# Performance work log

Hardware: AMD Instinct MI355X
Metric: run time of the kernel (lower is better)

Reference implementation:

```python
import jax, jax.numpy as jnp
import numpy as np

NUM_HEADS = 16
HEAD_DIM = 64
MAX_REL = 128
NEG_INF = -1e30


def setup_inputs() -> dict:
    key = jax.random.key(0)
    ks = jax.random.split(key, 5)
    B, L, D = 2, 2048, 1024
    x = jax.random.normal(ks[0], (B, L, D), dtype=jnp.float32)
    key_padding_mask = jnp.zeros((B, L), dtype=bool)  # True = padded
    Wqkv = jax.random.normal(ks[1], (D, 3 * D), dtype=jnp.float32) * (D ** -0.5)
    bqkv = jnp.zeros((3 * D,), dtype=jnp.float32)
    Wout = jax.random.normal(ks[2], (D, D), dtype=jnp.float32) * (D ** -0.5)
    bout = jnp.zeros((D,), dtype=jnp.float32)
    bias_table = jax.random.normal(ks[3], (2 * MAX_REL + 1, NUM_HEADS), dtype=jnp.float32) * 0.02
    return {"x": x, "key_padding_mask": key_padding_mask, "Wqkv": Wqkv,
            "bqkv": bqkv, "Wout": Wout, "bout": bout, "bias_table": bias_table}


def _rel_bias(bias_table, L):
    # relative position index: clamp(k - q, -MAX_REL, MAX_REL) + MAX_REL -> [L, L]
    rel = jnp.arange(L)[None, :] - jnp.arange(L)[:, None]
    idx = jnp.clip(rel, -MAX_REL, MAX_REL) + MAX_REL
    return bias_table[idx].transpose(2, 0, 1)  # [H, L, L]


def reference(x, key_padding_mask, Wqkv, bqkv, Wout, bout, bias_table):
    B, L, D = x.shape
    H, hd = NUM_HEADS, HEAD_DIM
    qkv = x @ Wqkv + bqkv                      # [B, L, 3D]
    q, k, v = jnp.split(qkv, 3, axis=-1)
    q = q.reshape(B, L, H, hd).transpose(0, 2, 1, 3)  # [B, H, L, hd]
    k = k.reshape(B, L, H, hd).transpose(0, 2, 1, 3)
    v = v.reshape(B, L, H, hd).transpose(0, 2, 1, 3)
    scores = jnp.einsum('bhqd,bhkd->bhqk', q, k) * (hd ** -0.5)
    scores = scores + _rel_bias(bias_table, L)[None]   # [B, H, L, L]
    scores = jnp.where(key_padding_mask[:, None, None, :], NEG_INF, scores)
    attn = jax.nn.softmax(scores, axis=-1)
    out = jnp.einsum('bhqk,bhkd->bhqd', attn, v)       # [B, H, L, hd]
    out = out.transpose(0, 2, 1, 3).reshape(B, L, D)
    return out @ Wout + bout
```

## Files before the change

### kernel.cpp

```cpp
#include <hip/hip_runtime.h>
#include <hip/hip_bf16.h>
#include <stdint.h>

#define LSEQ 2048
#define BATCH 2
#define DMODEL 1024
#define NH 16
#define HD 64

typedef __attribute__((ext_vector_type(8))) short bf16x8;
typedef __attribute__((ext_vector_type(4))) float f32x4;

__device__ __forceinline__ short f2bf(float f) {
  union { float f; uint32_t u; } v; v.f = f;
  uint32_t r = v.u + 0x8000u;
  return (short)(r >> 16);
}

__device__ __forceinline__ uint32_t pack_bf16(float lo, float hi) {
  union { float f; uint32_t u; } a, b; a.f = lo; b.f = hi;
  uint32_t al = (a.u + 0x8000u) >> 16;
  uint32_t bh = (b.u + 0x8000u) & 0xFFFF0000u;
  return al | bh;
}

__device__ __forceinline__ float exp2_fast(float x) {
#if __has_builtin(__builtin_amdgcn_exp2f)
  return __builtin_amdgcn_exp2f(x);
#else
  float r; asm("v_exp_f32 %0, %1" : "=v"(r) : "v"(x)); return r;
#endif
}

__device__ __forceinline__ void gll16(const void* g, void* l) {
  __builtin_amdgcn_global_load_lds(
      (const __attribute__((address_space(1))) void*)g,
      (__attribute__((address_space(3))) void*)l, 16, 0, 0);
}

__global__ void cvt_bf16(const float* __restrict__ in, short* __restrict__ out, int n) {
  int i = (blockIdx.x * blockDim.x + threadIdx.x) * 4;
  if (i < n) {
    float4 v = *(const float4*)(in + i);
    short4 o;
    o.x = f2bf(v.x); o.y = f2bf(v.y); o.z = f2bf(v.z); o.w = f2bf(v.w);
    *(short4*)(out + i) = o;
  }
}

__global__ void transpose_cvt(const float* __restrict__ in, short* __restrict__ out,
                              int K, int N) {
  __shared__ float tile[32][33];
  int kb = blockIdx.x * 32, nb = blockIdx.y * 32;
  int tx = threadIdx.x & 31, ty = threadIdx.x >> 5;
  #pragma unroll
  for (int i = ty; i < 32; i += 8)
    tile[i][tx] = in[(size_t)(kb + i) * N + nb + tx];
  __syncthreads();
  #pragma unroll
  for (int i = ty; i < 32; i += 8)
    out[(size_t)(nb + i) * K + kb + tx] = f2bf(tile[tx][i]);
}

template <int EPI>
__global__ __launch_bounds__(256, 2) void gemm_bt(
    const short* __restrict__ A, const short* __restrict__ Bt,
    const float* __restrict__ bias, float* __restrict__ outf,
    short* __restrict__ q_out, short* __restrict__ k_out, short* __restrict__ v_out) {
  constexpr int K = 1024, BK = 64, NKT = K / BK;
  __shared__ short Als[2][128 * BK];
  __shared__ short Bls[2][128 * BK];
  const int tid = threadIdx.x;
  const int lane = tid & 63;
  const int c = lane & 15, g = lane >> 4;
  const int m0 = blockIdx.x * 128;
  const int n0 = blockIdx.y * 128;
  const int wid = tid >> 6;
  const int wm = (wid >> 1) * 64, wn = (wid & 1) * 64;

  f32x4 acc[4][4] = {};

  auto stage = [&](int kt, int bbuf) {
    const int k0 = kt * BK;
    #pragma unroll
    for (int inst = 0; inst < 4; ++inst) {
      int i = inst * 256 + tid;
      int row = i >> 3, cg = i & 7;
      int scc = cg ^ (row & 7);
      gll16(A + (size_t)(m0 + row) * K + k0 + scc * 8, &Als[bbuf][i * 8]);
      gll16(Bt + (size_t)(n0 + row) * K + k0 + scc * 8, &Bls[bbuf][i * 8]);
    }
  };

  stage(0, 0);

  for (int kt = 0; kt < NKT; ++kt) {
    const int bb = kt & 1;
    asm volatile("s_waitcnt vmcnt(0)" ::: "memory");
    __builtin_amdgcn_s_barrier();
    if (kt < NKT - 1) stage(kt + 1, bb ^ 1);

    #pragma unroll
    for (int ks = 0; ks < 2; ++ks) {
      const int kb = ks * 64 + g * 16;
      bf16x8 af[4], bfv[4];
      #pragma unroll
      for (int m = 0; m < 4; ++m) {
        int row = wm + m * 16 + c;
        af[m] = *(const bf16x8*)((const char*)&Als[bb][0] + row * 128 + (kb ^ ((row & 7) << 4)));
      }
      #pragma unroll
      for (int n = 0; n < 4; ++n) {
        int row = wn + n * 16 + c;
        bfv[n] = *(const bf16x8*)((const char*)&Bls[bb][0] + row * 128 + (kb ^ ((row & 7) << 4)));
      }
      __builtin_amdgcn_s_setprio(1);
      #pragma unroll
      for (int m = 0; m < 4; ++m)
        #pragma unroll
        for (int n = 0; n < 4; ++n)
          acc[m][n] = __builtin_amdgcn_mfma_f32_16x16x32_bf16(af[m], bfv[n], acc[m][n], 0, 0, 0);
      __builtin_amdgcn_s_setprio(0);
    }
  }

  #pragma unroll
  for (int m = 0; m < 4; ++m) {
    #pragma unroll
    for (int n = 0; n < 4; ++n) {
      #pragma unroll
      for (int r = 0; r < 4; ++r) {
        int row = m0 + wm + m * 16 + g * 4 + r;
        int col = n0 + wn + n * 16 + c;
        float val = acc[m][n][r] + bias[col];
        if (EPI == 1) {
          outf[(size_t)row * DMODEL + col] = val;
        } else {
          int b = row >> 11, l = row & 2047;
          int which = col >> 10, rem = col & 1023;
          int hn = rem >> 6, d = rem & 63;
          size_t bh = (size_t)b * NH + hn;
          if (which == 0)       q_out[(bh * LSEQ + l) * HD + d] = f2bf(val * 0.1803368801f);
          else if (which == 1)  k_out[(bh * LSEQ + l) * HD + d] = f2bf(val);
          else                  v_out[(bh * HD + d) * LSEQ + l] = f2bf(val);
        }
      }
    }
  }
}

__global__ __launch_bounds__(256, 2) void attn_kernel(
    const short* __restrict__ qb, const short* __restrict__ kb,
    const short* __restrict__ vtb, const unsigned char* __restrict__ kpm,
    const float* __restrict__ bias_table, short* __restrict__ ob) {
  constexpr int NT = LSEQ / 64;
  __shared__ short Kls[2][64 * 64];
  __shared__ short Vls[2][64 * 64];
  __shared__ short Pls[4][32 * 64];
  __shared__ float biasc[257];
  __shared__ unsigned mbits_s;

  const int tid = threadIdx.x, lane = tid & 63, wid = tid >> 6;
  const int g = lane >> 4, c = lane & 15;
  const int lin = blockIdx.x;
  const int swz = (lin & 7) * 64 + (lin >> 3);
  const int q0 = (swz & 15) * 128;
  const int h = (swz >> 4) & 15;
  const int b = swz >> 8;
  const size_t bh = (size_t)b * NH + h;
  const short* qbase = qb + bh * LSEQ * HD;
  const short* kbase = kb + bh * LSEQ * HD;
  const short* vbase = vtb + bh * HD * LSEQ;
  const unsigned char* kpmb = kpm + (size_t)b * LSEQ;

  bf16x8 qf[2][2];
  #pragma unroll
  for (int qg = 0; qg < 2; ++qg)
    #pragma unroll
    for (int ks = 0; ks < 2; ++ks) {
      int qrow = q0 + wid * 32 + qg * 16 + c;
      qf[qg][ks] = *(const bf16x8*)(qbase + (size_t)qrow * HD + ks * 32 + g * 8);
    }

  if (tid < 32) {
    const uint4* mp = (const uint4*)(kpmb + tid * 64);
    uint4 m0 = mp[0], m1 = mp[1], m2 = mp[2], m3 = mp[3];
    unsigned anyb = m0.x | m0.y | m0.z | m0.w | m1.x | m1.y | m1.z | m1.w |
                    m2.x | m2.y | m2.z | m2.w | m3.x | m3.y | m3.z | m3.w;
    unsigned long long bal = __ballot(anyb != 0);
    if (tid == 0) mbits_s = (unsigned)bal;
  }
  for (int i = tid; i < 257; i += 256) biasc[i] = bias_table[i * NH + h] * 1.44269504f;
  __syncthreads();
  const unsigned mbits = mbits_s;
  const float cb_lo = biasc[0], cb_hi = biasc[256];

  auto stage = [&](int t, int bbuf) {
    const int kv0s = t * 64;
    #pragma unroll
    for (int inst = 0; inst < 2; ++inst) {
      int cc0 = inst * 256 + tid;
      int row = cc0 >> 3, cc = cc0 & 7;
      int scc = cc ^ (row & 7);
      gll16(kbase + (size_t)(kv0s + row) * HD + scc * 8, &Kls[bbuf][cc0 * 8]);
      gll16(vbase + (size_t)row * LSEQ + kv0s + scc * 8, &Vls[bbuf][cc0 * 8]);
    }
  };

  f32x4 o[4][2], l_acc[2];
  #pragma unroll
  for (int nt = 0; nt < 4; ++nt)
    #pragma unroll
    for (int qg = 0; qg < 2; ++qg) o[nt][qg] = (f32x4){0.f, 0.f, 0.f, 0.f};
  l_acc[0] = (f32x4){0.f, 0.f, 0.f, 0.f};
  l_acc[1] = (f32x4){0.f, 0.f, 0.f, 0.f};

  bf16x8 onesf;
  #pragma unroll
  for (int j = 0; j < 8; ++j) onesf[j] = (short)0x3F80;

  char* pw = (char*)&Pls[wid][0];
  const int c7s = (c & 7) << 4;

  stage(0, 0);

  for (int t = 0; t < NT; ++t) {
    const int bb = t & 1;
    const int kv0 = t * 64;
    asm volatile("s_waitcnt vmcnt(0)" ::: "memory");
    __builtin_amdgcn_s_barrier();
    if (t < NT - 1) stage(t + 1, bb ^ 1);

    f32x4 st[4][2];
    __builtin_amdgcn_s_setprio(1);
    #pragma unroll
    for (int nt = 0; nt < 4; ++nt) {
      f32x4 a0 = {}, a1 = {};
      #pragma unroll
      for (int ks = 0; ks < 2; ++ks) {
        int krow = nt * 16 + c;
        int kbyte = ks * 64 + g * 16;
        const bf16x8 kf =
            *(const bf16x8*)((const char*)&Kls[bb][0] + krow * 128 + (kbyte ^ c7s));
        a0 = __builtin_amdgcn_mfma_f32_16x16x32_bf16(kf, qf[0][ks], a0, 0, 0, 0);
        a1 = __builtin_amdgcn_mfma_f32_16x16x32_bf16(kf, qf[1][ks], a1, 0, 0, 0);
      }
      st[nt][0] = a0; st[nt][1] = a1;
    }
    __builtin_amdgcn_s_setprio(0);

    const int dw = kv0 - q0 - wid * 32;
    if (dw >= 160 || dw <= -192) {
      const float cb = dw > 0 ? cb_hi : cb_lo;
      #pragma unroll
      for (int nt = 0; nt < 4; ++nt)
        #pragma unroll
        for (int qg = 0; qg < 2; ++qg)
          #pragma unroll
          for (int r = 0; r < 4; ++r) st[nt][qg][r] += cb;
    } else {
      #pragma unroll
      for (int nt = 0; nt < 4; ++nt)
        #pragma unroll
        for (int qg = 0; qg < 2; ++qg) {
          const int base = dw + nt * 16 + g * 4 - qg * 16 - c;
          #pragma unroll
          for (int r = 0; r < 4; ++r) {
            int rel = base + r;
            rel = rel < -128 ? -128 : (rel > 128 ? 128 : rel);
            st[nt][qg][r] += biasc[rel + 128];
          }
        }
    }
    if (mbits & (1u << t)) {
      #pragma unroll
      for (int nt = 0; nt < 4; ++nt)
        #pragma unroll
        for (int r = 0; r < 4; ++r) {
          float mk = kpmb[kv0 + nt * 16 + g * 4 + r] ? -1e30f : 0.f;
          st[nt][0][r] += mk;
          st[nt][1][r] += mk;
        }
    }

    #pragma unroll
    for (int qg = 0; qg < 2; ++qg)
      #pragma unroll
      for (int nt = 0; nt < 4; ++nt) {
        uint32_t p01 = pack_bf16(exp2_fast(st[nt][qg][0]), exp2_fast(st[nt][qg][1]));
        uint32_t p23 = pack_bf16(exp2_fast(st[nt][qg][2]), exp2_fast(st[nt][qg][3]));
        uint2 w; w.x = p01; w.y = p23;
        *(uint2*)(pw + (qg * 16 + c) * 128 + ((nt * 32 + g * 8) ^ c7s)) = w;
      }

    asm volatile("s_waitcnt lgkmcnt(0)" ::: "memory");
    __builtin_amdgcn_sched_barrier(0);

    __builtin_amdgcn_s_setprio(1);
    #pragma unroll
    for (int ks = 0; ks < 2; ++ks) {
      const int pbyte = ks * 64 + g * 16;
      bf16x8 pa0 = *(const bf16x8*)(pw + c * 128 + (pbyte ^ c7s));
      bf16x8 pa1 = *(const bf16x8*)(pw + (16 + c) * 128 + (pbyte ^ c7s));
      l_acc[0] = __builtin_amdgcn_mfma_f32_16x16x32_bf16(pa0, onesf, l_acc[0], 0, 0, 0);
      l_acc[1] = __builtin_amdgcn_mfma_f32_16x16x32_bf16(pa1, onesf, l_acc[1], 0, 0, 0);
      #pragma unroll
      for (int nt = 0; nt < 4; ++nt) {
        int vrow = nt * 16 + c;
        const bf16x8 vf =
            *(const bf16x8*)((const char*)&Vls[bb][0] + vrow * 128 + (pbyte ^ c7s));
        o[nt][0] = __builtin_amdgcn_mfma_f32_16x16x32_bf16(pa0, vf, o[nt][0], 0, 0, 0);
        o[nt][1] = __builtin_amdgcn_mfma_f32_16x16x32_bf16(pa1, vf, o[nt][1], 0, 0, 0);
      }
    }
    __builtin_amdgcn_s_setprio(0);
  }

  #pragma unroll
  for (int qg = 0; qg < 2; ++qg)
    #pragma unroll
    for (int r = 0; r < 4; ++r) {
      float inv = 1.f / l_acc[qg][r];
      int qrow = q0 + wid * 32 + qg * 16 + g * 4 + r;
      size_t obase = ((size_t)b * LSEQ + qrow) * DMODEL + (size_t)h * HD;
      #pragma unroll
      for (int nt = 0; nt < 4; ++nt)
        ob[obase + nt * 16 + c] = f2bf(o[nt][qg][r] * inv);
    }
}

extern "C" void kernel_launch(void* const* d_in, const int* in_sizes, int n_in,
                              void* d_out, int out_size, void* d_ws, size_t ws_size,
                              hipStream_t stream) {
  (void)in_sizes; (void)n_in; (void)out_size; (void)ws_size;
  const float* x = (const float*)d_in[0];
  const unsigned char* kpm = (const unsigned char*)d_in[1];
  const float* Wqkv = (const float*)d_in[2];
  const float* bqkv = (const float*)d_in[3];
  const float* Wout = (const float*)d_in[4];
  const float* bout = (const float*)d_in[5];
  const float* btab = (const float*)d_in[6];
  float* out = (float*)d_out;

  short* ws = (short*)d_ws;
  short* xbf   = ws;
  short* wqkvT = xbf + 4194304;
  short* woutT = wqkvT + 3145728;
  short* qbuf  = woutT + 1048576;
  short* kbuf  = qbuf + 4194304;
  short* vtbuf = kbuf + 4194304;
  short* obuf  = vtbuf + 4194304;

  cvt_bf16<<<dim3(4096), dim3(256), 0, stream>>>(x, xbf, 4194304);
  transpose_cvt<<<dim3(32, 96), dim3(256), 0, stream>>>(Wqkv, wqkvT, 1024, 3072);
  transpose_cvt<<<dim3(32, 32), dim3(256), 0, stream>>>(Wout, woutT, 1024, 1024);

  gemm_bt<0><<<dim3(32, 24), dim3(256), 0, stream>>>(xbf, wqkvT, bqkv, nullptr,
                                                     qbuf, kbuf, vtbuf);
  attn_kernel<<<dim3(512), dim3(256), 0, stream>>>(qbuf, kbuf, vtbuf, kpm, btab, obuf);
  gemm_bt<1><<<dim3(32, 8), dim3(256), 0, stream>>>(obuf, woutT, bout, out,
                                                    nullptr, nullptr, nullptr);
}
```

Baseline: 136.4 us.

## Merge prep kernels into one launch and retype P tile LDS access

Replaces the three separate conversion/transpose launches with a single prep kernel that dispatches on block index, removing two kernel launches. In attention, the P tile in LDS is retyped as uint2 so stores and loads are 8-byte pieces with an XOR swizzle. The explicit lgkmcnt wait, sched barrier and priority drop around the PV MFMAs are removed, leaving the compiler to order them. Removing the explicit wait risks different instruction scheduling, and the 8-byte loads may need more LDS instructions than the 16-byte reads.

```diff
diff --git a/kernel.cpp b/kernel.cpp
--- a/kernel.cpp
+++ b/kernel.cpp
@@ -38,20 +38,23 @@
       (__attribute__((address_space(3))) void*)l, 16, 0, 0);
 }
 
-__global__ void cvt_bf16(const float* __restrict__ in, short* __restrict__ out, int n) {
-  int i = (blockIdx.x * blockDim.x + threadIdx.x) * 4;
-  if (i < n) {
-    float4 v = *(const float4*)(in + i);
+__global__ void prep_kernel(const float* __restrict__ x, const float* __restrict__ Wqkv,
+                            const float* __restrict__ Wout, short* __restrict__ xbf,
+                            short* __restrict__ wqkvT, short* __restrict__ woutT) {
+  __shared__ float tile[32][33];
+  const int bid = blockIdx.x;
+  if (bid < 4096) {
+    int i = (bid * 256 + threadIdx.x) * 4;
+    float4 v = *(const float4*)(x + i);
     short4 o;
     o.x = f2bf(v.x); o.y = f2bf(v.y); o.z = f2bf(v.z); o.w = f2bf(v.w);
-    *(short4*)(out + i) = o;
-  }
-}
-
-__global__ void transpose_cvt(const float* __restrict__ in, short* __restrict__ out,
-                              int K, int N) {
-  __shared__ float tile[32][33];
-  int kb = blockIdx.x * 32, nb = blockIdx.y * 32;
+    *(short4*)(xbf + i) = o;
+    return;
+  }
+  const float* in; short* out; int K, N, t;
+  if (bid < 7168) { in = Wqkv; out = wqkvT; K = 1024; N = 3072; t = bid - 4096; }
+  else            { in = Wout; out = woutT; K = 1024; N = 1024; t = bid - 7168; }
+  int kb = (t & 31) * 32, nb = (t >> 5) * 32;
   int tx = threadIdx.x & 31, ty = threadIdx.x >> 5;
   #pragma unroll
   for (int i = ty; i < 32; i += 8)
@@ -156,7 +159,7 @@
   constexpr int NT = LSEQ / 64;
   __shared__ short Kls[2][64 * 64];
   __shared__ short Vls[2][64 * 64];
-  __shared__ short Pls[4][32 * 64];
+  __shared__ uint2 Pls[4][512];
   __shared__ float biasc[257];
   __shared__ unsigned mbits_s;
 
@@ -219,8 +222,9 @@
   #pragma unroll
   for (int j = 0; j < 8; ++j) onesf[j] = (short)0x3F80;
 
-  char* pw = (char*)&Pls[wid][0];
+  uint2* pw = &Pls[wid][0];
   const int c7s = (c & 7) << 4;
+  const int cx  = (c & 7) << 1;
 
   stage(0, 0);
 
@@ -287,23 +291,22 @@
     for (int qg = 0; qg < 2; ++qg)
       #pragma unroll
       for (int nt = 0; nt < 4; ++nt) {
-        uint32_t p01 = pack_bf16(exp2_fast(st[nt][qg][0]), exp2_fast(st[nt][qg][1]));
-        uint32_t p23 = pack_bf16(exp2_fast(st[nt][qg][2]), exp2_fast(st[nt][qg][3]));
-        uint2 w; w.x = p01; w.y = p23;
-        *(uint2*)(pw + (qg * 16 + c) * 128 + ((nt * 32 + g * 8) ^ c7s)) = w;
-      }
-
-    asm volatile("s_waitcnt lgkmcnt(0)" ::: "memory");
-    __builtin_amdgcn_sched_barrier(0);
-
-    __builtin_amdgcn_s_setprio(1);
+        uint2 w;
+        w.x = pack_bf16(exp2_fast(st[nt][qg][0]), exp2_fast(st[nt][qg][1]));
+        w.y = pack_bf16(exp2_fast(st[nt][qg][2]), exp2_fast(st[nt][qg][3]));
+        pw[(qg * 16 + c) * 16 + ((nt * 4 + g) ^ cx)] = w;
+      }
+
     #pragma unroll
     for (int ks = 0; ks < 2; ++ks) {
-      const int pbyte = ks * 64 + g * 16;
-      bf16x8 pa0 = *(const bf16x8*)(pw + c * 128 + (pbyte ^ c7s));
-      bf16x8 pa1 = *(const bf16x8*)(pw + (16 + c) * 128 + (pbyte ^ c7s));
+      const int pu = (ks * 8 + g * 2) ^ cx;
+      union { uint2 u[2]; bf16x8 v; } pa0u, pa1u;
+      pa0u.u[0] = pw[c * 16 + pu];        pa0u.u[1] = pw[c * 16 + pu + 1];
+      pa1u.u[0] = pw[(16 + c) * 16 + pu]; pa1u.u[1] = pw[(16 + c) * 16 + pu + 1];
+      const bf16x8 pa0 = pa0u.v, pa1 = pa1u.v;
       l_acc[0] = __builtin_amdgcn_mfma_f32_16x16x32_bf16(pa0, onesf, l_acc[0], 0, 0, 0);
       l_acc[1] = __builtin_amdgcn_mfma_f32_16x16x32_bf16(pa1, onesf, l_acc[1], 0, 0, 0);
+      const int pbyte = ks * 64 + g * 16;
       #pragma unroll
       for (int nt = 0; nt < 4; ++nt) {
         int vrow = nt * 16 + c;
@@ -313,7 +316,6 @@
         o[nt][1] = __builtin_amdgcn_mfma_f32_16x16x32_bf16(pa1, vf, o[nt][1], 0, 0, 0);
       }
     }
-    __builtin_amdgcn_s_setprio(0);
   }
 
   #pragma unroll
@@ -351,9 +353,7 @@
   short* vtbuf = kbuf + 4194304;
   short* obuf  = vtbuf + 4194304;
 
-  cvt_bf16<<<dim3(4096), dim3(256), 0, stream>>>(x, xbf, 4194304);
-  transpose_cvt<<<dim3(32, 96), dim3(256), 0, stream>>>(Wqkv, wqkvT, 1024, 3072);
-  transpose_cvt<<<dim3(32, 32), dim3(256), 0, stream>>>(Wout, woutT, 1024, 1024);
+  prep_kernel<<<dim3(8192), dim3(256), 0, stream>>>(x, Wqkv, Wout, xbf, wqkvT, woutT);
 
   gemm_bt<0><<<dim3(32, 24), dim3(256), 0, stream>>>(xbf, wqkvT, bqkv, nullptr,
                                                      qbuf, kbuf, vtbuf);
```

Result: faster. 131.6 us (median of 2 runs) (-3.5%).
